# Kernel tuning notes

Hardware: AMD Instinct MI355X
Metric: run time of the kernel (lower is better)

Reference implementation:

```python
import jax, jax.numpy as jnp
import numpy as np

EMBED_DIM = 1024
NUM_HEADS = 16
HEAD_DIM = EMBED_DIM // NUM_HEADS


def setup_inputs() -> dict:
    key = jax.random.key(0)
    ks = jax.random.split(key, 9)
    B, S, E = 4, 2048, EMBED_DIM
    # xavier_uniform bound for square [E, E] weights
    bound = float(np.sqrt(6.0 / (E + E)))
    def w(k):
        return jax.random.uniform(k, (E, E), jnp.float32, -bound, bound)
    return {
        "x": jax.random.normal(ks[0], (B, S, E), jnp.float32),
        "Wq": w(ks[1]), "bq": jnp.zeros((E,), jnp.float32),
        "Wk": w(ks[2]), "bk": jnp.zeros((E,), jnp.float32),
        "Wv": w(ks[3]), "bv": jnp.zeros((E,), jnp.float32),
        "Wo": w(ks[4]), "bo": jnp.zeros((E,), jnp.float32),
    }


def reference(x, Wq, bq, Wk, bk, Wv, bv, Wo, bo):
    B, S, E = x.shape
    H, D = NUM_HEADS, HEAD_DIM
    # Linear projections (torch Linear: x @ W.T + b)
    q = (x @ Wq.T + bq).reshape(B, S, H, D)
    k = (x @ Wk.T + bk).reshape(B, S, H, D)
    v = (x @ Wv.T + bv).reshape(B, S, H, D)
    # per-head scaled dot-product attention (vectorized over heads)
    scores = jnp.einsum("bqhd,bkhd->bhqk", q, k) / jnp.sqrt(jnp.float32(D))
    attn = jax.nn.softmax(scores, axis=-1)
    o = jnp.einsum("bhqk,bkhd->bqhd", attn, v).reshape(B, S, E)
    return o @ Wo.T + bo
```

## Files before the change

### kernel.cpp

```cpp
#include <hip/hip_runtime.h>
#include <stdint.h>

typedef unsigned short u16;
typedef short bf16x8 __attribute__((ext_vector_type(8)));
typedef float f32x4 __attribute__((ext_vector_type(4)));
typedef float f32x16 __attribute__((ext_vector_type(16)));

#define B_ 4
#define S_ 2048
#define H_ 16
#define D_ 64
#define E_ 1024
#define M_ (B_ * S_)

static __device__ __forceinline__ u16 f2bf(float f) {
  uint32_t u = __builtin_bit_cast(uint32_t, f);
  u += 0x7fffu + ((u >> 16) & 1u);
  return (u16)(u >> 16);
}
static __device__ __forceinline__ uint32_t pack2bf(float a, float b) {
  return (uint32_t)f2bf(a) | ((uint32_t)f2bf(b) << 16);
}
static __device__ __forceinline__ uint32_t cvt_pk_bf16(float a, float b) {
  uint32_t r;
  asm("v_cvt_pk_bf16_f32 %0, %1, %2" : "=v"(r) : "v"(a), "v"(b));
  return r;
}
static __device__ __forceinline__ void pl32swap(uint32_t& a, uint32_t& b) {
  asm volatile("v_permlane32_swap_b32 %0, %1" : "+v"(a), "+v"(b));
}

static __device__ __forceinline__ void gld_lds16(const void* g, void* l) {
  __builtin_amdgcn_global_load_lds(
      (const __attribute__((address_space(1))) void*)(uintptr_t)g,
      (__attribute__((address_space(3))) void*)(uint32_t)(uintptr_t)l, 16, 0, 0);
}

__global__ __launch_bounds__(256) void cvt_f32_bf16(const float* __restrict__ in,
                                                    u16* __restrict__ out, int n) {
  int i = (blockIdx.x * 256 + threadIdx.x) * 8;
  if (i + 8 > n) return;
  float4 a = *(const float4*)(in + i);
  float4 b = *(const float4*)(in + i + 4);
  struct __align__(16) U8 { u16 h[8]; } u;
  u.h[0] = f2bf(a.x); u.h[1] = f2bf(a.y); u.h[2] = f2bf(a.z); u.h[3] = f2bf(a.w);
  u.h[4] = f2bf(b.x); u.h[5] = f2bf(b.y); u.h[6] = f2bf(b.z); u.h[7] = f2bf(b.w);
  *(U8*)(out + i) = u;
}

template <int KIND, typename OutT>
static __device__ __forceinline__ void gemm128(const u16* __restrict__ A,
                                               const u16* __restrict__ W,
                                               const float* __restrict__ bias,
                                               OutT* __restrict__ C, int m0, int n0,
                                               float scale, u16* As, u16* Bs) {
  const int tid = threadIdx.x;
  const int wave = tid >> 6, lane = tid & 63;
  const int col16 = lane & 15, quad = lane >> 4;
  const int wm = wave >> 1, wn = wave & 1;

  f32x4 acc[4][4] = {};

  const int r0 = tid >> 3;
  const int sg8 = ((tid & 7) ^ (r0 & 7)) * 8;
  const u16* ga = A + (size_t)(m0 + r0) * E_ + sg8;
  const u16* gb = W + (size_t)(n0 + r0) * E_ + sg8;
  u16* lA = As + wave * 512;
  u16* lB = Bs + wave * 512;

  auto stage = [&](int k0, int buf) {
#pragma unroll
    for (int i = 0; i < 4; i++) {
      gld_lds16(ga + (size_t)(i * 32) * E_ + k0, lA + buf * 8192 + i * 2048);
      gld_lds16(gb + (size_t)(i * 32) * E_ + k0, lB + buf * 8192 + i * 2048);
    }
  };

  stage(0, 0);
  const int NK = E_ / 64;
  for (int kk = 0; kk < NK; kk++) {
    asm volatile("s_waitcnt vmcnt(0)" ::: "memory");
    __builtin_amdgcn_s_barrier();
    if (kk + 1 < NK) stage((kk + 1) * 64, (kk + 1) & 1);

    const u16* AsC = As + (kk & 1) * 8192;
    const u16* BsC = Bs + (kk & 1) * 8192;

    bf16x8 af[4][2], bw[4][2];
#pragma unroll
    for (int mt = 0; mt < 4; mt++)
#pragma unroll
      for (int ks = 0; ks < 2; ks++)
        af[mt][ks] = *(const bf16x8*)&AsC[(wm * 64 + mt * 16 + col16) * 64 +
                                          (((ks * 4 + quad) ^ (col16 & 7)) * 8)];
#pragma unroll
    for (int nt = 0; nt < 4; nt++)
#pragma unroll
      for (int ks = 0; ks < 2; ks++)
        bw[nt][ks] = *(const bf16x8*)&BsC[(wn * 64 + nt * 16 + col16) * 64 +
                                          (((ks * 4 + quad) ^ (col16 & 7)) * 8)];
#pragma unroll
    for (int ks = 0; ks < 2; ks++)
#pragma unroll
      for (int a = 0; a < 4; a++)
#pragma unroll
        for (int b = 0; b < 4; b++) {
          if constexpr (KIND == 2)
            acc[a][b] = __builtin_amdgcn_mfma_f32_16x16x32_bf16(af[a][ks], bw[b][ks], acc[a][b], 0, 0, 0);
          else
            acc[a][b] = __builtin_amdgcn_mfma_f32_16x16x32_bf16(bw[a][ks], af[b][ks], acc[a][b], 0, 0, 0);
        }
  }

  if constexpr (KIND == 2) {
#pragma unroll
    for (int a = 0; a < 4; a++) {
      int t = m0 + wm * 64 + a * 16 + quad * 4;
      int bb = t >> 11, s = t & (S_ - 1);
#pragma unroll
      for (int b = 0; b < 4; b++) {
        int oc = n0 + wn * 64 + b * 16 + col16;
        int h = oc >> 6, d = oc & 63;
        float bv = bias[oc];
        uint32_t lo = pack2bf(acc[a][b][0] + bv, acc[a][b][1] + bv);
        uint32_t hi = pack2bf(acc[a][b][2] + bv, acc[a][b][3] + bv);
        uint2 pk = {lo, hi};
        *(uint2*)&C[(((size_t)(bb * H_ + h) * D_ + d) * S_) + s] = pk;
      }
    }
  } else {
#pragma unroll
    for (int b = 0; b < 4; b++) {
      int row = m0 + wm * 64 + b * 16 + col16;
#pragma unroll
      for (int a = 0; a < 4; a++) {
        int nc = n0 + wn * 64 + a * 16 + quad * 4;
        float4 bv = *(const float4*)&bias[nc];
        float v0 = (acc[a][b][0] + bv.x) * scale;
        float v1 = (acc[a][b][1] + bv.y) * scale;
        float v2 = (acc[a][b][2] + bv.z) * scale;
        float v3 = (acc[a][b][3] + bv.w) * scale;
        if constexpr (KIND == 0) {
          uint2 pk = {pack2bf(v0, v1), pack2bf(v2, v3)};
          *(uint2*)&((u16*)C)[(size_t)row * E_ + nc] = pk;
        } else {
          float4 pk = {v0, v1, v2, v3};
          *(float4*)&((float*)C)[(size_t)row * E_ + nc] = pk;
        }
      }
    }
  }
}

__global__ __launch_bounds__(256) void gemm_qkv(const u16* __restrict__ xb,
                                                const u16* __restrict__ wq, const u16* __restrict__ wk,
                                                const u16* __restrict__ wv,
                                                const float* __restrict__ bq, const float* __restrict__ bk,
                                                const float* __restrict__ bv,
                                                u16* __restrict__ Qb, u16* __restrict__ Kb,
                                                u16* __restrict__ Vtb) {
  __shared__ __align__(16) u16 As[2][128 * 64];
  __shared__ __align__(16) u16 Bs[2][128 * 64];
  const int mat = blockIdx.x >> 3;
  const int n0 = (blockIdx.x & 7) * 128;
  const int m0 = blockIdx.y * 128;
  if (mat == 0)
    gemm128<0, u16>(xb, wq, bq, Qb, m0, n0, 0.125f * 1.44269504f, &As[0][0], &Bs[0][0]);
  else if (mat == 1)
    gemm128<0, u16>(xb, wk, bk, Kb, m0, n0, 1.0f, &As[0][0], &Bs[0][0]);
  else
    gemm128<2, u16>(xb, wv, bv, Vtb, m0, n0, 1.0f, &As[0][0], &Bs[0][0]);
}

__global__ __launch_bounds__(256) void gemm_out(const u16* __restrict__ Ob,
                                                const u16* __restrict__ wob,
                                                const float* __restrict__ bo,
                                                float* __restrict__ out) {
  __shared__ __align__(16) u16 As[2][128 * 64];
  __shared__ __align__(16) u16 Bs[2][128 * 64];
  gemm128<1, float>(Ob, wob, bo, out, blockIdx.y * 128, blockIdx.x * 128, 1.0f,
                    &As[0][0], &Bs[0][0]);
}

__global__ __launch_bounds__(512) void flash_attn(const u16* __restrict__ Q,
                                                  const u16* __restrict__ K,
                                                  const u16* __restrict__ Vt,
                                                  u16* __restrict__ O) {
  __shared__ __align__(16) u16 Ks[3][64 * 64];
  __shared__ __align__(16) u16 Vs[3][64 * 64];
  const int bid = blockIdx.x;
  const int qt = bid & 7, h = (bid >> 3) & 15, b = bid >> 7;
  const int tid = threadIdx.x;
  const int wave = tid >> 6, lane = tid & 63;
  const int l31 = lane & 31, hi = lane >> 5;
  const int sw7 = l31 & 7;

  const int srow = tid >> 3;
  const int sgrp = (tid & 7) ^ (srow & 7);
  const u16* Kbase = K + ((size_t)(b * S_) * H_ + h) * D_;
  const u16* Vbase = Vt + ((size_t)(b * H_ + h) * D_) * S_;

  auto stage = [&](int kb, int buf) {
    gld_lds16(Kbase + (size_t)(kb * 64 + srow) * (H_ * D_) + sgrp * 8,
              &Ks[buf][wave * 512]);
    gld_lds16(Vbase + (size_t)srow * S_ + kb * 64 + sgrp * 8,
              &Vs[buf][wave * 512]);
  };

  stage(0, 0);
  stage(1, 1);

  const int qrow = qt * 256 + wave * 32;
  bf16x8 qf[4];
  const u16* qp = Q + ((size_t)(b * S_ + qrow + l31) * H_ + h) * D_ + hi * 8;
#pragma unroll
  for (int t = 0; t < 4; t++) qf[t] = *(const bf16x8*)(qp + t * 16);

  f32x16 o_acc[2] = {};
  float l_sum = 0.f;

  const int NT = S_ / 64;
  int cur = 0;
  for (int kb = 0; kb < NT; kb++) {
    if (kb + 1 < NT)
      asm volatile("s_waitcnt vmcnt(2)" ::: "memory");
    else
      asm volatile("s_waitcnt vmcnt(0)" ::: "memory");
    __builtin_amdgcn_s_barrier();
    if (kb + 2 < NT) {
      int nb = cur + 2; if (nb >= 3) nb -= 3;
      stage(kb + 2, nb);
    }
    const u16* KsC = Ks[cur];
    const u16* VsC = Vs[cur];

#pragma unroll
    for (int kblk = 0; kblk < 2; kblk++) {
      const int krow = kblk * 32 + l31;
      const int ksw = krow & 7;
      f32x16 sacc = {};
      __builtin_amdgcn_s_setprio(1);
#pragma unroll
      for (int t = 0; t < 4; t++) {
        bf16x8 kf = *(const bf16x8*)&KsC[krow * 64 + (((2 * t + hi) ^ ksw) * 8)];
        sacc = __builtin_amdgcn_mfma_f32_32x32x16_bf16(kf, qf[t], sacc, 0, 0, 0);
      }
      __builtin_amdgcn_s_setprio(0);

      float p[16];
#pragma unroll
      for (int e = 0; e < 16; e++) p[e] = __builtin_amdgcn_exp2f(sacc[e]);
      float s0 = (p[0] + p[1]) + (p[2] + p[3]);
      float s1 = (p[4] + p[5]) + (p[6] + p[7]);
      float s2 = (p[8] + p[9]) + (p[10] + p[11]);
      float s3 = (p[12] + p[13]) + (p[14] + p[15]);
      l_sum += (s0 + s1) + (s2 + s3);
      uint32_t W[8];
#pragma unroll
      for (int i = 0; i < 8; i++) W[i] = cvt_pk_bf16(p[2 * i], p[2 * i + 1]);

#pragma unroll
      for (int kf2 = 0; kf2 < 2; kf2++) {
        uint32_t w0 = W[kf2 * 4 + 0], w1 = W[kf2 * 4 + 1];
        uint32_t w2 = W[kf2 * 4 + 2], w3 = W[kf2 * 4 + 3];
        pl32swap(w0, w2);
        pl32swap(w1, w3);
        union { uint32_t w[4]; bf16x8 v; } u;
        u.w[0] = w0; u.w[1] = w1; u.w[2] = w2; u.w[3] = w3;
        const bf16x8 pa = u.v;
        const int kf = kblk * 2 + kf2;
        __builtin_amdgcn_s_setprio(1);
#pragma unroll
        for (int n = 0; n < 2; n++) {
          const int dr = n * 32 + l31;
          bf16x8 vf = *(const bf16x8*)&VsC[dr * 64 + (((2 * kf + hi) ^ sw7) * 8)];
          o_acc[n] = __builtin_amdgcn_mfma_f32_32x32x16_bf16(pa, vf, o_acc[n], 0, 0, 0);
        }
        __builtin_amdgcn_s_setprio(0);
      }
    }
    cur = (cur + 1 == 3) ? 0 : cur + 1;
  }

  float l_tot = l_sum + __shfl_xor(l_sum, 32);
  float inv = 1.f / l_tot;

#pragma unroll
  for (int r = 0; r < 16; r++) {
    const int ql = (r & 3) + 8 * (r >> 2) + 4 * hi;
    const float iq = __shfl(inv, ql);
    u16* op = O + ((size_t)(b * S_ + qrow + ql) * H_ + h) * D_ + l31;
#pragma unroll
    for (int n = 0; n < 2; n++) op[n * 32] = f2bf(o_acc[n][r] * iq);
  }
}

extern "C" void kernel_launch(void* const* d_in, const int* in_sizes, int n_in,
                              void* d_out, int out_size, void* d_ws, size_t ws_size,
                              hipStream_t stream) {
  (void)in_sizes; (void)n_in; (void)out_size; (void)ws_size;
  const float* x  = (const float*)d_in[0];
  const float* Wq = (const float*)d_in[1];
  const float* bq = (const float*)d_in[2];
  const float* Wk = (const float*)d_in[3];
  const float* bk = (const float*)d_in[4];
  const float* Wv = (const float*)d_in[5];
  const float* bv = (const float*)d_in[6];
  const float* Wo = (const float*)d_in[7];
  const float* bo = (const float*)d_in[8];
  float* out = (float*)d_out;

  const size_t NX = (size_t)M_ * E_;
  const size_t NW = (size_t)E_ * E_;
  u16* xb  = (u16*)d_ws;
  u16* wqb = xb + NX;
  u16* wkb = wqb + NW;
  u16* wvb = wkb + NW;
  u16* wob = wvb + NW;
  u16* Qb  = wob + NW;
  u16* Kb  = Qb + NX;
  u16* Vtb = Kb + NX;
  u16* Ob  = Vtb + NX;

  cvt_f32_bf16<<<NX / 2048, 256, 0, stream>>>(x, xb, (int)NX);
  cvt_f32_bf16<<<NW / 2048, 256, 0, stream>>>(Wq, wqb, (int)NW);
  cvt_f32_bf16<<<NW / 2048, 256, 0, stream>>>(Wk, wkb, (int)NW);
  cvt_f32_bf16<<<NW / 2048, 256, 0, stream>>>(Wv, wvb, (int)NW);
  cvt_f32_bf16<<<NW / 2048, 256, 0, stream>>>(Wo, wob, (int)NW);

  gemm_qkv<<<dim3(24, 64), 256, 0, stream>>>(xb, wqb, wkb, wvb, bq, bk, bv, Qb, Kb, Vtb);
  flash_attn<<<B_ * H_ * (S_ / 256), 512, 0, stream>>>(Qb, Kb, Vtb, Ob);
  gemm_out<<<dim3(8, 64), 256, 0, stream>>>(Ob, wob, bo, out);
}
```

Baseline: 275.9 us.

## Double-buffer 128-key attention tiles and merge weight conversions into one launch

The attention kernel moves from a triple-buffered 64-key pipeline with partial vmcnt waits to a double-buffered scheme that stages 128 keys per round, so there is one barrier and one full wait per 128 keys. The four weight fp32-to-bf16 conversion launches become a single kernel that picks its source by block index, removing three launches. In exchange, prefetch depth drops to one round ahead and each round waits for all outstanding loads, which may expose more memory latency. LDS use rises from 3 to 4 tiles each for K and V.

```diff
diff --git a/kernel.cpp b/kernel.cpp
--- a/kernel.cpp
+++ b/kernel.cpp
@@ -46,6 +46,23 @@
   u.h[0] = f2bf(a.x); u.h[1] = f2bf(a.y); u.h[2] = f2bf(a.z); u.h[3] = f2bf(a.w);
   u.h[4] = f2bf(b.x); u.h[5] = f2bf(b.y); u.h[6] = f2bf(b.z); u.h[7] = f2bf(b.w);
   *(U8*)(out + i) = u;
+}
+
+__global__ __launch_bounds__(256) void cvt_w4(const float* __restrict__ w0,
+                                              const float* __restrict__ w1,
+                                              const float* __restrict__ w2,
+                                              const float* __restrict__ w3,
+                                              u16* __restrict__ out) {
+  const int NW_BLK = (E_ * E_) / 2048;
+  const int seg = blockIdx.x >> 9;
+  const float* src = seg == 0 ? w0 : seg == 1 ? w1 : seg == 2 ? w2 : w3;
+  int i = ((blockIdx.x & (NW_BLK - 1)) * 256 + threadIdx.x) * 8;
+  float4 a = *(const float4*)(src + i);
+  float4 b = *(const float4*)(src + i + 4);
+  struct __align__(16) U8 { u16 h[8]; } u;
+  u.h[0] = f2bf(a.x); u.h[1] = f2bf(a.y); u.h[2] = f2bf(a.z); u.h[3] = f2bf(a.w);
+  u.h[4] = f2bf(b.x); u.h[5] = f2bf(b.y); u.h[6] = f2bf(b.z); u.h[7] = f2bf(b.w);
+  *(U8*)(out + (size_t)seg * (E_ * E_) + i) = u;
 }
 
 template <int KIND, typename OutT>
@@ -186,8 +203,8 @@
                                                   const u16* __restrict__ K,
                                                   const u16* __restrict__ Vt,
                                                   u16* __restrict__ O) {
-  __shared__ __align__(16) u16 Ks[3][64 * 64];
-  __shared__ __align__(16) u16 Vs[3][64 * 64];
+  __shared__ __align__(16) u16 Ks[2][2][64 * 64];
+  __shared__ __align__(16) u16 Vs[2][2][64 * 64];
   const int bid = blockIdx.x;
   const int qt = bid & 7, h = (bid >> 3) & 15, b = bid >> 7;
   const int tid = threadIdx.x;
@@ -200,15 +217,17 @@
   const u16* Kbase = K + ((size_t)(b * S_) * H_ + h) * D_;
   const u16* Vbase = Vt + ((size_t)(b * H_ + h) * D_) * S_;
 
-  auto stage = [&](int kb, int buf) {
-    gld_lds16(Kbase + (size_t)(kb * 64 + srow) * (H_ * D_) + sgrp * 8,
-              &Ks[buf][wave * 512]);
-    gld_lds16(Vbase + (size_t)srow * S_ + kb * 64 + sgrp * 8,
-              &Vs[buf][wave * 512]);
+  auto stage = [&](int r, int buf) {
+#pragma unroll
+    for (int sub = 0; sub < 2; sub++) {
+      gld_lds16(Kbase + (size_t)(r * 128 + sub * 64 + srow) * (H_ * D_) + sgrp * 8,
+                &Ks[buf][sub][wave * 512]);
+      gld_lds16(Vbase + (size_t)srow * S_ + r * 128 + sub * 64 + sgrp * 8,
+                &Vs[buf][sub][wave * 512]);
+    }
   };
 
   stage(0, 0);
-  stage(1, 1);
 
   const int qrow = qt * 256 + wave * 32;
   bf16x8 qf[4];
@@ -219,30 +238,24 @@
   f32x16 o_acc[2] = {};
   float l_sum = 0.f;
 
-  const int NT = S_ / 64;
-  int cur = 0;
-  for (int kb = 0; kb < NT; kb++) {
-    if (kb + 1 < NT)
-      asm volatile("s_waitcnt vmcnt(2)" ::: "memory");
-    else
-      asm volatile("s_waitcnt vmcnt(0)" ::: "memory");
+  const int NR = S_ / 128;
+  for (int r = 0; r < NR; r++) {
+    asm volatile("s_waitcnt vmcnt(0)" ::: "memory");
     __builtin_amdgcn_s_barrier();
-    if (kb + 2 < NT) {
-      int nb = cur + 2; if (nb >= 3) nb -= 3;
-      stage(kb + 2, nb);
-    }
-    const u16* KsC = Ks[cur];
-    const u16* VsC = Vs[cur];
-
-#pragma unroll
-    for (int kblk = 0; kblk < 2; kblk++) {
-      const int krow = kblk * 32 + l31;
-      const int ksw = krow & 7;
+    if (r + 1 < NR) stage(r + 1, (r + 1) & 1);
+    const u16* KsC = &Ks[r & 1][0][0];
+    const u16* VsC = &Vs[r & 1][0][0];
+
+#pragma unroll
+    for (int kblk = 0; kblk < 4; kblk++) {
+      const u16* Ksub = KsC + (kblk >> 1) * 4096;
+      const u16* Vsub = VsC + (kblk >> 1) * 4096;
+      const int krow = (kblk & 1) * 32 + l31;
       f32x16 sacc = {};
       __builtin_amdgcn_s_setprio(1);
 #pragma unroll
       for (int t = 0; t < 4; t++) {
-        bf16x8 kf = *(const bf16x8*)&KsC[krow * 64 + (((2 * t + hi) ^ ksw) * 8)];
+        bf16x8 kf = *(const bf16x8*)&Ksub[krow * 64 + (((2 * t + hi) ^ sw7) * 8)];
         sacc = __builtin_amdgcn_mfma_f32_32x32x16_bf16(kf, qf[t], sacc, 0, 0, 0);
       }
       __builtin_amdgcn_s_setprio(0);
@@ -268,18 +281,17 @@
         union { uint32_t w[4]; bf16x8 v; } u;
         u.w[0] = w0; u.w[1] = w1; u.w[2] = w2; u.w[3] = w3;
         const bf16x8 pa = u.v;
-        const int kf = kblk * 2 + kf2;
+        const int kfs = (kblk & 1) * 2 + kf2;
         __builtin_amdgcn_s_setprio(1);
 #pragma unroll
         for (int n = 0; n < 2; n++) {
           const int dr = n * 32 + l31;
-          bf16x8 vf = *(const bf16x8*)&VsC[dr * 64 + (((2 * kf + hi) ^ sw7) * 8)];
+          bf16x8 vf = *(const bf16x8*)&Vsub[dr * 64 + (((2 * kfs + hi) ^ sw7) * 8)];
           o_acc[n] = __builtin_amdgcn_mfma_f32_32x32x16_bf16(pa, vf, o_acc[n], 0, 0, 0);
         }
         __builtin_amdgcn_s_setprio(0);
       }
     }
-    cur = (cur + 1 == 3) ? 0 : cur + 1;
   }
 
   float l_tot = l_sum + __shfl_xor(l_sum, 32);
@@ -323,10 +335,7 @@
   u16* Ob  = Vtb + NX;
 
   cvt_f32_bf16<<<NX / 2048, 256, 0, stream>>>(x, xb, (int)NX);
-  cvt_f32_bf16<<<NW / 2048, 256, 0, stream>>>(Wq, wqb, (int)NW);
-  cvt_f32_bf16<<<NW / 2048, 256, 0, stream>>>(Wk, wkb, (int)NW);
-  cvt_f32_bf16<<<NW / 2048, 256, 0, stream>>>(Wv, wvb, (int)NW);
-  cvt_f32_bf16<<<NW / 2048, 256, 0, stream>>>(Wo, wob, (int)NW);
+  cvt_w4<<<4 * (NW / 2048), 256, 0, stream>>>(Wq, Wk, Wv, Wo, wqb);
 
   gemm_qkv<<<dim3(24, 64), 256, 0, stream>>>(xb, wqb, wkb, wvb, bq, bk, bv, Qb, Kb, Vtb);
   flash_attn<<<B_ * H_ * (S_ / 256), 512, 0, stream>>>(Qb, Kb, Vtb, Ob);
```

Result: no change. 275.0 us (-0.3%).
